# Kernel tuning notes

Hardware: AMD Instinct MI355X
Metric: run time of the kernel (lower is better)

Reference implementation:

```python
import jax, jax.numpy as jnp
import numpy as np

N_NODES = 100000
N_EDGES = 1600000
N_GRAPHS = 2000
F_IN = 64
HID = 64


def setup_inputs() -> dict:
    key = jax.random.key(0)
    ks = jax.random.split(key, 8)
    h = jax.random.normal(ks[0], (N_NODES, F_IN), jnp.float32)
    edge_src = jax.random.randint(ks[1], (N_EDGES,), 0, N_NODES, jnp.int32)
    edge_dst = jax.random.randint(ks[2], (N_EDGES,), 0, N_NODES, jnp.int32)
    graph_ids = jnp.sort(jax.random.randint(ks[3], (N_NODES,), 0, N_GRAPHS, jnp.int32))
    # GraphConv weights (glorot-ish scale) and biases, 3 layers 64->64
    sc = 1.0 / np.sqrt(F_IN)
    W0 = jax.random.normal(ks[4], (F_IN, HID), jnp.float32) * sc
    W1 = jax.random.normal(ks[5], (HID, HID), jnp.float32) * sc
    W2 = jax.random.normal(ks[6], (HID, HID), jnp.float32) * sc
    b0 = jnp.zeros((HID,), jnp.float32)
    b1 = jnp.zeros((HID,), jnp.float32)
    b2 = jnp.zeros((HID,), jnp.float32)
    return dict(h=h, edge_src=edge_src, edge_dst=edge_dst, graph_ids=graph_ids,
                W0=W0, b0=b0, W1=W1, b1=b1, W2=W2, b2=b2)


def _gcn_layer(h, W, b, src, dst, out_deg_isqrt, in_deg_isqrt, apply_relu):
    # DGL GraphConv, norm='both': D_in^{-1/2} A D_out^{-1/2} h W + b
    hw = (h * out_deg_isqrt[:, None]) @ W          # weight/norm commute with sum
    m = jax.ops.segment_sum(hw[src], dst, num_segments=N_NODES)  # gather->scatter-add
    m = m * in_deg_isqrt[:, None] + b
    return jax.nn.relu(m) if apply_relu else m


def reference(h, edge_src, edge_dst, graph_ids, W0, b0, W1, b1, W2, b2):
    ones = jnp.ones((N_EDGES,), h.dtype)
    out_deg = jnp.clip(jax.ops.segment_sum(ones, edge_src, num_segments=N_NODES), 1.0, None)
    in_deg = jnp.clip(jax.ops.segment_sum(ones, edge_dst, num_segments=N_NODES), 1.0, None)
    odi = jax.lax.rsqrt(out_deg)
    idi = jax.lax.rsqrt(in_deg)
    params = [(W0, b0), (W1, b1), (W2, b2)]
    for i, (W, b) in enumerate(params):
        h = _gcn_layer(h, W, b, edge_src, edge_dst, odi, idi, apply_relu=(i < len(params) - 1))
    # self.factor = sqrt(dim) / mean(||h||) computed as python float -> detached constant
    factor = jnp.sqrt(jnp.asarray(HID, h.dtype)) / jnp.mean(jnp.linalg.norm(h, axis=1))
    factor = jax.lax.stop_gradient(factor)
    h = h * factor
    # SumPooling over batched graphs
    return jax.ops.segment_sum(h, graph_ids, num_segments=N_GRAPHS)
```

## Files before the change

kernel.cpp:

```cpp
#include <hip/hip_runtime.h>
#include <hip/hip_fp16.h>

#define N_NODES 100000
#define N_EDGES 1600000
#define N_GRAPHS 2000
#define HID 64
#define NB 391
#define CAP 5120
#define NSUP 16
#define SUPW 6400
#define CAP_S 106496
#define CH_A 2048
#define NCH_A ((N_EDGES + CH_A - 1) / CH_A)
#define BCH 4096
#define NCHB 26
#define GATHER_GRID 2048
#define GEMM_GRID 512
#define N_GROUPS (N_NODES / 4)
#define N_TILE16 (N_NODES / 16)

typedef _Float16 half8 __attribute__((ext_vector_type(8)));
typedef float f32x4 __attribute__((ext_vector_type(4)));

__global__ __launch_bounds__(256) void k_zero2(int* __restrict__ p1, int n1,
                                               int* __restrict__ p2, int n2) {
    int i = blockIdx.x * 256 + threadIdx.x;
    if (i < n1) p1[i] = 0;
    if (i < n2) p2[i] = 0;
}

__global__ __launch_bounds__(256) void k_passA(const int* __restrict__ src, const int* __restrict__ dst,
                                               int* __restrict__ scur_dst, int* __restrict__ scur_src,
                                               unsigned* __restrict__ sup_dst,
                                               unsigned short* __restrict__ sup_src) {
    __shared__ unsigned stD[CH_A];
    __shared__ unsigned short stS[CH_A];
    __shared__ unsigned char binD[CH_A];
    __shared__ unsigned char binS[CH_A];
    __shared__ int lcntD[NSUP], lexD[NSUP], lofD[NSUP], runD[NSUP];
    __shared__ int lcntS[NSUP], lexS[NSUP], lofS[NSUP], runS[NSUP];
    int tid = threadIdx.x;
    int e0 = blockIdx.x * CH_A;
    int n = min(CH_A, N_EDGES - e0);
    if (tid < NSUP) { lcntD[tid] = 0; lcntS[tid] = 0; }
    __syncthreads();
    int sv[8], dv[8];
#pragma unroll
    for (int k = 0; k < 8; ++k) {
        int i = k * 256 + tid;
        if (i < n) { sv[k] = src[e0 + i]; dv[k] = dst[e0 + i]; }
        else dv[k] = -1;
    }
#pragma unroll
    for (int k = 0; k < 8; ++k)
        if (dv[k] >= 0) {
            atomicAdd(&lcntD[dv[k] / SUPW], 1);
            atomicAdd(&lcntS[sv[k] / SUPW], 1);
        }
    __syncthreads();
    if (tid == 0)  { int a = 0; for (int i = 0; i < NSUP; ++i) { lexD[i] = a; lofD[i] = a; a += lcntD[i]; } }
    if (tid == 64) { int a = 0; for (int i = 0; i < NSUP; ++i) { lexS[i] = a; lofS[i] = a; a += lcntS[i]; } }
    __syncthreads();
#pragma unroll
    for (int k = 0; k < 8; ++k)
        if (dv[k] >= 0) {
            int d = dv[k], s = sv[k];
            int bD = d / SUPW;
            int pD = atomicAdd(&lofD[bD], 1);
            stD[pD] = ((unsigned)(d - bD * SUPW) << 17) | (unsigned)s;
            binD[pD] = (unsigned char)bD;
            int bS = s / SUPW;
            int pS = atomicAdd(&lofS[bS], 1);
            stS[pS] = (unsigned short)(s - bS * SUPW);
            binS[pS] = (unsigned char)bS;
        }
    __syncthreads();
    if (tid < NSUP) runD[tid] = lcntD[tid] ? atomicAdd(&scur_dst[tid], lcntD[tid]) : 0;
    if (tid >= 128 && tid < 128 + NSUP) {
        int b = tid - 128;
        runS[b] = lcntS[b] ? atomicAdd(&scur_src[b], lcntS[b]) : 0;
    }
    __syncthreads();
    for (int i = tid; i < n; i += 256) {
        int b = binD[i];
        int pos = runD[b] + (i - lexD[b]);
        if (pos < CAP_S) sup_dst[(size_t)b * CAP_S + pos] = stD[i];
    }
    for (int i = tid; i < n; i += 256) {
        int b = binS[i];
        int pos = runS[b] + (i - lexS[b]);
        if (pos < CAP_S) sup_src[(size_t)b * CAP_S + pos] = stS[i];
    }
}

__global__ __launch_bounds__(256) void k_passB(const unsigned* __restrict__ sup_dst,
                                               const unsigned short* __restrict__ sup_src,
                                               const int* __restrict__ scur_dst,
                                               const int* __restrict__ scur_src,
                                               int* __restrict__ gcur_dst, int* __restrict__ gcur_src,
                                               unsigned* __restrict__ part_dst,
                                               unsigned char* __restrict__ part_src) {
    __shared__ unsigned st[BCH];
    __shared__ unsigned char bin[BCH];
    __shared__ int lcnt[25], lex[25], lof[25], run[25];
    int tid = threadIdx.x;
    int isSrc = blockIdx.x >= NSUP * NCHB;
    int bx = isSrc ? blockIdx.x - NSUP * NCHB : blockIdx.x;
    int sb = bx / NCHB, ch = bx % NCHB;
    int total = isSrc ? scur_src[sb] : scur_dst[sb];
    total = min(total, CAP_S);
    int o0 = ch * BCH;
    int n = min(BCH, total - o0);
    if (n <= 0) return;
    int bg0 = sb * 25;
    if (tid < 25) lcnt[tid] = 0;
    __syncthreads();

    if (!isSrc) {
        unsigned ev[16];
        int bb[16];
#pragma unroll
        for (int k = 0; k < 16; ++k) {
            int i = k * 256 + tid;
            if (i < n) {
                unsigned e = sup_dst[(size_t)sb * CAP_S + o0 + i];
                ev[k] = e;
                bb[k] = (int)(e >> 25);
                atomicAdd(&lcnt[bb[k]], 1);
            } else bb[k] = -1;
        }
        __syncthreads();
        if (tid == 0) { int a = 0; for (int i = 0; i < 25; ++i) { lex[i] = a; lof[i] = a; a += lcnt[i]; } }
        __syncthreads();
#pragma unroll
        for (int k = 0; k < 16; ++k)
            if (bb[k] >= 0) {
                unsigned e = ev[k];
                unsigned s = e & 0x1FFFFu;
                unsigned low = (e >> 17) & 255u;
                int p = atomicAdd(&lof[bb[k]], 1);
                st[p] = (s << 8) | low;
                bin[p] = (unsigned char)bb[k];
            }
        __syncthreads();
        if (tid < 25) run[tid] = lcnt[tid] ? atomicAdd(&gcur_dst[bg0 + tid], lcnt[tid]) : 0;
        __syncthreads();
        for (int i = tid; i < n; i += 256) {
            int b = bin[i];
            int pos = run[b] + (i - lex[b]);
            if (pos < CAP) part_dst[(size_t)(bg0 + b) * CAP + pos] = st[i];
        }
    } else {
        unsigned char* st8 = (unsigned char*)st;
        int rv[16];
        int bb[16];
#pragma unroll
        for (int k = 0; k < 16; ++k) {
            int i = k * 256 + tid;
            if (i < n) {
                int r = (int)sup_src[(size_t)sb * CAP_S + o0 + i];
                rv[k] = r;
                bb[k] = r >> 8;
                atomicAdd(&lcnt[bb[k]], 1);
            } else bb[k] = -1;
        }
        __syncthreads();
        if (tid == 0) { int a = 0; for (int i = 0; i < 25; ++i) { lex[i] = a; lof[i] = a; a += lcnt[i]; } }
        __syncthreads();
#pragma unroll
        for (int k = 0; k < 16; ++k)
            if (bb[k] >= 0) {
                int p = atomicAdd(&lof[bb[k]], 1);
                st8[p] = (unsigned char)(rv[k] & 255);
                bin[p] = (unsigned char)bb[k];
            }
        __syncthreads();
        if (tid < 25) run[tid] = lcnt[tid] ? atomicAdd(&gcur_src[bg0 + tid], lcnt[tid]) : 0;
        __syncthreads();
        for (int i = tid; i < n; i += 256) {
            int b = bin[i];
            int pos = run[b] + (i - lex[b]);
            if (pos < CAP) part_src[(size_t)(bg0 + b) * CAP + pos] = st8[i];
        }
    }
}

__global__ __launch_bounds__(256) void k_csr_count(const unsigned* __restrict__ part_dst,
                                                   const unsigned char* __restrict__ part_src,
                                                   const int* __restrict__ gcur_dst,
                                                   const int* __restrict__ gcur_src,
                                                   int* __restrict__ rowbeg, int* __restrict__ rowend,
                                                   float* __restrict__ idi, float* __restrict__ odi,
                                                   int* __restrict__ col) {
    __shared__ int cnt[256];
    __shared__ int cur[256];
    __shared__ int wsum[4];
    int tid = threadIdx.x;
    if (blockIdx.x >= NB) {
        int b = blockIdx.x - NB;
        int nE = min(gcur_src[b], CAP);
        const unsigned char* pb = part_src + (size_t)b * CAP;
        cnt[tid] = 0;
        __syncthreads();
        for (int i = tid; i < nE; i += 256) atomicAdd(&cnt[pb[i]], 1);
        __syncthreads();
        int v = b * 256 + tid;
        if (v < N_NODES) odi[v] = rsqrtf((float)max(cnt[tid], 1));
        return;
    }
    int b = blockIdx.x;
    int base = b * CAP;
    int nE = min(gcur_dst[b], CAP);
    const unsigned* pb = part_dst + (size_t)b * CAP;
    cnt[tid] = 0;
    __syncthreads();
    for (int i = tid; i < nE; i += 256) atomicAdd(&cnt[pb[i] & 255], 1);
    __syncthreads();
    int c = cnt[tid];
    int incl = c;
#pragma unroll
    for (int off = 1; off < 64; off <<= 1) {
        int t = __shfl_up(incl, off, 64);
        if ((tid & 63) >= off) incl += t;
    }
    if ((tid & 63) == 63) wsum[tid >> 6] = incl;
    __syncthreads();
    int add = 0;
    for (int w = 0; w < (tid >> 6); ++w) add += wsum[w];
    incl += add;
    int excl = incl - c;
    int v = b * 256 + tid;
    if (v < N_NODES) {
        rowbeg[v] = base + excl;
        rowend[v] = base + incl;
        idi[v] = rsqrtf((float)max(c, 1));
    }
    cur[tid] = excl;
    __syncthreads();
    for (int i = tid; i < nE; i += 256) {
        unsigned e = pb[i];
        int p = atomicAdd(&cur[e & 255], 1);
        col[base + p] = (int)(e >> 8);
    }
}

template <int F32IN>
__global__ __launch_bounds__(256) void k_gemm_mfma(const void* __restrict__ inv,
                                                   const float* __restrict__ W,
                                                   const float* __restrict__ odi,
                                                   __half* __restrict__ zs) {
    __shared__ _Float16 Wt[64 * 64];
    int tid = threadIdx.x;
    for (int i = tid; i < 4096; i += 256) {
        int k = i >> 6, j = i & 63;
        Wt[j * 64 + k] = (_Float16)W[i];
    }
    __syncthreads();

    int lane = tid & 63;
    int wid = tid >> 6;
    int lrow = lane & 15;
    int lgrp = lane >> 4;

    half8 Bf[4][2];
#pragma unroll
    for (int nt = 0; nt < 4; ++nt)
#pragma unroll
        for (int kh = 0; kh < 2; ++kh)
            Bf[nt][kh] = *(half8*)&Wt[(nt * 16 + lrow) * 64 + kh * 32 + lgrp * 8];

    for (int t = blockIdx.x * 4 + wid; t < N_TILE16; t += GEMM_GRID * 4) {
        int v0 = t * 16;
        half8 a0, a1;
        if (F32IN) {
            const float* A = (const float*)inv + (size_t)(v0 + lrow) * 64 + lgrp * 8;
            float4 f0 = *(const float4*)A;
            float4 f1 = *(const float4*)(A + 4);
            float4 g0 = *(const float4*)(A + 32);
            float4 g1 = *(const float4*)(A + 36);
            a0[0] = (_Float16)f0.x; a0[1] = (_Float16)f0.y; a0[2] = (_Float16)f0.z; a0[3] = (_Float16)f0.w;
            a0[4] = (_Float16)f1.x; a0[5] = (_Float16)f1.y; a0[6] = (_Float16)f1.z; a0[7] = (_Float16)f1.w;
            a1[0] = (_Float16)g0.x; a1[1] = (_Float16)g0.y; a1[2] = (_Float16)g0.z; a1[3] = (_Float16)g0.w;
            a1[4] = (_Float16)g1.x; a1[5] = (_Float16)g1.y; a1[6] = (_Float16)g1.z; a1[7] = (_Float16)g1.w;
        } else {
            const _Float16* A = (const _Float16*)inv + (size_t)(v0 + lrow) * 64 + lgrp * 8;
            a0 = *(const half8*)A;
            a1 = *(const half8*)(A + 32);
        }
        f32x4 acc[4];
#pragma unroll
        for (int nt = 0; nt < 4; ++nt) { acc[nt] = (f32x4)0.f; }
#pragma unroll
        for (int nt = 0; nt < 4; ++nt) {
            acc[nt] = __builtin_amdgcn_mfma_f32_16x16x32_f16(a0, Bf[nt][0], acc[nt], 0, 0, 0);
            acc[nt] = __builtin_amdgcn_mfma_f32_16x16x32_f16(a1, Bf[nt][1], acc[nt], 0, 0, 0);
        }
#pragma unroll
        for (int r = 0; r < 4; ++r) {
            int node = v0 + lgrp * 4 + r;
            float w = odi[node];
#pragma unroll
            for (int nt = 0; nt < 4; ++nt)
                zs[(size_t)node * 64 + nt * 16 + lrow] = __float2half_rn(acc[nt][r] * w);
        }
    }
}

template <int RELU, int LAST>
__global__ __launch_bounds__(256) void k_gather(const __half* __restrict__ zs, const int* __restrict__ rowbeg,
                                                const int* __restrict__ rowend, const int* __restrict__ col,
                                                const float* __restrict__ idi, const float* __restrict__ b,
                                                __half* __restrict__ xout, float* __restrict__ partials) {
    __shared__ float part[4];
    int tid = threadIdx.x;
    int lane = tid & 63;
    int wid = tid >> 6;
    int half = lane >> 5;
    int fp = lane & 31;
    float2 bias2 = *(const float2*)&b[fp * 2];
    float nacc = 0.f;

    for (int g = blockIdx.x; g < N_GROUPS; g += GATHER_GRID) {
        int v = __builtin_amdgcn_readfirstlane(g * 4 + wid);
        int beg = rowbeg[v], end = rowend[v];
        int deg = end - beg;
        int degS = min(deg, 64);
        int c = col[beg + min(lane, max(degS - 1, 0))];
        float2 a0 = {0.f, 0.f}, a1 = {0.f, 0.f}, a2 = {0.f, 0.f}, a3 = {0.f, 0.f};
        int m = 0;
        for (; (m + 8) * 2 <= degS; m += 8) {
#pragma unroll
            for (int j = 0; j < 8; ++j) {
                int s = __shfl(c, 2 * (m + j) + half, 64);
                float2 f = __half22float2(*((const __half2*)(zs + (size_t)s * 64) + fp));
                if ((j & 3) == 0) { a0.x += f.x; a0.y += f.y; }
                else if ((j & 3) == 1) { a1.x += f.x; a1.y += f.y; }
                else if ((j & 3) == 2) { a2.x += f.x; a2.y += f.y; }
                else { a3.x += f.x; a3.y += f.y; }
            }
        }
        if ((m + 4) * 2 <= degS) {
#pragma unroll
            for (int j = 0; j < 4; ++j) {
                int s = __shfl(c, 2 * (m + j) + half, 64);
                float2 f = __half22float2(*((const __half2*)(zs + (size_t)s * 64) + fp));
                if (j == 0) { a0.x += f.x; a0.y += f.y; }
                else if (j == 1) { a1.x += f.x; a1.y += f.y; }
                else if (j == 2) { a2.x += f.x; a2.y += f.y; }
                else { a3.x += f.x; a3.y += f.y; }
            }
            m += 4;
        }
        if (m * 2 < degS) {
#pragma unroll
            for (int j = 0; j < 4; ++j) {
                int e = 2 * (m + j) + half;
                int ee = (e < degS) ? e : (degS - 1);
                int s = __shfl(c, ee, 64);
                float2 f = __half22float2(*((const __half2*)(zs + (size_t)s * 64) + fp));
                float msk = (e < degS) ? 1.f : 0.f;
                if (j == 0) { a0.x = fmaf(f.x, msk, a0.x); a0.y = fmaf(f.y, msk, a0.y); }
                else if (j == 1) { a1.x = fmaf(f.x, msk, a1.x); a1.y = fmaf(f.y, msk, a1.y); }
                else if (j == 2) { a2.x = fmaf(f.x, msk, a2.x); a2.y = fmaf(f.y, msk, a2.y); }
                else { a3.x = fmaf(f.x, msk, a3.x); a3.y = fmaf(f.y, msk, a3.y); }
            }
        }
        if (deg > 64) {
            for (int p = beg + 64; p < end; p += 8) {
#pragma unroll
                for (int j = 0; j < 4; ++j) {
                    int e = p + 2 * j + half;
                    int q = (e < end) ? e : (end - 1);
                    int s = col[q];
                    float2 f = __half22float2(*((const __half2*)(zs + (size_t)s * 64) + fp));
                    float msk = (e < end) ? 1.f : 0.f;
                    a0.x = fmaf(f.x, msk, a0.x); a0.y = fmaf(f.y, msk, a0.y);
                }
            }
        }
        float2 a;
        a.x = (a0.x + a1.x) + (a2.x + a3.x);
        a.y = (a0.y + a1.y) + (a2.y + a3.y);
        a.x += __shfl_xor(a.x, 32, 64);
        a.y += __shfl_xor(a.y, 32, 64);
        float iv = idi[v];
        float2 o;
        o.x = fmaf(a.x, iv, bias2.x);
        o.y = fmaf(a.y, iv, bias2.y);
        if (RELU) { o.x = fmaxf(o.x, 0.f); o.y = fmaxf(o.y, 0.f); }

        if (half == 0)
            *((__half2*)(xout + (size_t)v * 64) + fp) = __floats2half2_rn(o.x, o.y);

        if (LAST) {
            float s = o.x * o.x + o.y * o.y;
#pragma unroll
            for (int off = 32; off > 0; off >>= 1) s += __shfl_xor(s, off, 64);
            if (lane == 0) nacc += sqrtf(0.5f * s);
        }
    }

    if (LAST) {
        if (lane == 0) part[wid] = nacc;
        __syncthreads();
        if (tid == 0) partials[blockIdx.x] = part[0] + part[1] + part[2] + part[3];
    }
}

__global__ __launch_bounds__(256) void k_reduce_factor(const float* __restrict__ partials,
                                                       float* __restrict__ factor) {
    __shared__ float sd[256];
    int tid = threadIdx.x;
    float s = 0.f;
    for (int i = tid; i < GATHER_GRID; i += 256) s += partials[i];
    sd[tid] = s;
    __syncthreads();
    for (int off = 128; off > 0; off >>= 1) {
        if (tid < off) sd[tid] += sd[tid + off];
        __syncthreads();
    }
    if (tid == 0) factor[0] = 8.0f * (float)N_NODES / sd[0];
}

#define POOL_CHUNK 32
__global__ __launch_bounds__(256) void k_pool(const __half* __restrict__ h, const int* __restrict__ gid,
                                              const float* __restrict__ factor, float* __restrict__ out) {
    int wave = (blockIdx.x * 256 + threadIdx.x) >> 6;
    int lane = threadIdx.x & 63;
    int v0 = wave * POOL_CHUNK;
    if (v0 >= N_NODES) return;
    float f = factor[0];
    int vend = min(v0 + POOL_CHUNK, N_NODES);
    int gprev = gid[v0];
    float acc = 0.f;
    for (int v = v0; v < vend; ++v) {
        int g = gid[v];
        if (g != gprev) {
            atomicAdd(&out[(size_t)gprev * 64 + lane], acc);
            acc = 0.f;
            gprev = g;
        }
        acc = fmaf(__half2float(h[(size_t)v * 64 + lane]), f, acc);
    }
    atomicAdd(&out[(size_t)gprev * 64 + lane], acc);
}

extern "C" void kernel_launch(void* const* d_in, const int* in_sizes, int n_in,
                              void* d_out, int out_size, void* d_ws, size_t ws_size,
                              hipStream_t stream) {
    const float* h    = (const float*)d_in[0];
    const int*   esrc = (const int*)d_in[1];
    const int*   edst = (const int*)d_in[2];
    const int*   gids = (const int*)d_in[3];
    const float* W0 = (const float*)d_in[4];
    const float* b0 = (const float*)d_in[5];
    const float* W1 = (const float*)d_in[6];
    const float* b1 = (const float*)d_in[7];
    const float* W2 = (const float*)d_in[8];
    const float* b2 = (const float*)d_in[9];
    float* out = (float*)d_out;

    char* wsp = (char*)d_ws;
    size_t off = 0;
    auto alloc = [&](size_t bytes) -> void* {
        void* p = wsp + off;
        off += (bytes + 255) & ~(size_t)255;
        return p;
    };
    int*   cursors    = (int*)alloc(814 * 4);
    float* odi        = (float*)alloc((size_t)N_NODES * 4);
    float* idi        = (float*)alloc((size_t)N_NODES * 4);
    int*   rowbeg     = (int*)alloc((size_t)N_NODES * 4);
    int*   rowend     = (int*)alloc((size_t)N_NODES * 4);
    float* partials   = (float*)alloc((size_t)GATHER_GRID * 4);
    float* factor     = (float*)alloc(4);
    int*   col        = (int*)alloc((size_t)NB * CAP * 4);
    __half* zsb       = (__half*)alloc((size_t)N_NODES * 64 * 2);
    __half* xh        = (__half*)alloc((size_t)N_NODES * 64 * 2);
    unsigned*       sup_dst  = (unsigned*)alloc((size_t)NSUP * CAP_S * 4);
    unsigned short* sup_src  = (unsigned short*)alloc((size_t)NSUP * CAP_S * 2);
    unsigned*       part_dst = (unsigned*)alloc((size_t)NB * CAP * 4);
    unsigned char*  part_src = (unsigned char*)alloc((size_t)NB * CAP);

    int* scur_dst = cursors;
    int* scur_src = cursors + 16;
    int* gcur_dst = cursors + 32;
    int* gcur_src = cursors + 32 + NB;

    k_zero2<<<(N_GRAPHS * 64 + 255) / 256, 256, 0, stream>>>(cursors, 814, (int*)out, N_GRAPHS * 64);

    k_passA<<<NCH_A, 256, 0, stream>>>(esrc, edst, scur_dst, scur_src, sup_dst, sup_src);
    k_passB<<<2 * NSUP * NCHB, 256, 0, stream>>>(sup_dst, sup_src, scur_dst, scur_src,
                                                 gcur_dst, gcur_src, part_dst, part_src);
    k_csr_count<<<2 * NB, 256, 0, stream>>>(part_dst, part_src, gcur_dst, gcur_src,
                                            rowbeg, rowend, idi, odi, col);

    k_gemm_mfma<1><<<GEMM_GRID, 256, 0, stream>>>(h, W0, odi, zsb);
    k_gather<1, 0><<<GATHER_GRID, 256, 0, stream>>>(zsb, rowbeg, rowend, col, idi, b0, xh, nullptr);
    k_gemm_mfma<0><<<GEMM_GRID, 256, 0, stream>>>(xh, W1, odi, zsb);
    k_gather<1, 0><<<GATHER_GRID, 256, 0, stream>>>(zsb, rowbeg, rowend, col, idi, b1, xh, nullptr);
    k_gemm_mfma<0><<<GEMM_GRID, 256, 0, stream>>>(xh, W2, odi, zsb);
    k_gather<0, 1><<<GATHER_GRID, 256, 0, stream>>>(zsb, rowbeg, rowend, col, idi, b2, xh, partials);

    k_reduce_factor<<<1, 256, 0, stream>>>(partials, factor);
    int poolWaves  = (N_NODES + POOL_CHUNK - 1) / POOL_CHUNK;
    int poolBlocks = (poolWaves + 3) / 4;
    k_pool<<<poolBlocks, 256, 0, stream>>>(xh, gids, factor, out);
}
```

Measured before the change: 206.5 us.

## Fuse sum pooling into last gather layer and scale output in finish kernel

The final aggregation layer now adds its per-node outputs directly into per-graph accumulators with atomics, instead of writing fp16 node features for a separate pooling kernel to read back. Because pooling is linear, the norm factor is applied afterwards by a finish kernel in which every block redundantly reduces the partial norms and scales its slice of the output. Every gather layer also switches from interleaved 4-node groups to contiguous 13-node runs per wave, which lets consecutive nodes of one graph share an accumulator. The cost is some load imbalance from the fixed chunks and a small repeated reduction in each finish block.

```diff
diff --git a/kernel.cpp b/kernel.cpp
--- a/kernel.cpp
+++ b/kernel.cpp
@@ -15,8 +15,8 @@
 #define BCH 4096
 #define NCHB 26
 #define GATHER_GRID 2048
+#define NPW 13
 #define GEMM_GRID 512
-#define N_GROUPS (N_NODES / 4)
 #define N_TILE16 (N_NODES / 16)
 
 typedef _Float16 half8 __attribute__((ext_vector_type(8)));
@@ -310,7 +310,8 @@
 __global__ __launch_bounds__(256) void k_gather(const __half* __restrict__ zs, const int* __restrict__ rowbeg,
                                                 const int* __restrict__ rowend, const int* __restrict__ col,
                                                 const float* __restrict__ idi, const float* __restrict__ b,
-                                                __half* __restrict__ xout, float* __restrict__ partials) {
+                                                __half* __restrict__ xout, const int* __restrict__ gid,
+                                                float* __restrict__ out, float* __restrict__ partials) {
     __shared__ float part[4];
     int tid = threadIdx.x;
     int lane = tid & 63;
@@ -319,9 +320,14 @@
     int fp = lane & 31;
     float2 bias2 = *(const float2*)&b[fp * 2];
     float nacc = 0.f;
-
-    for (int g = blockIdx.x; g < N_GROUPS; g += GATHER_GRID) {
-        int v = __builtin_amdgcn_readfirstlane(g * 4 + wid);
+    float2 pacc = {0.f, 0.f};
+    int curg = -1;
+
+    int w = __builtin_amdgcn_readfirstlane(blockIdx.x * 4 + wid);
+    int v0 = w * NPW;
+    int vend = min(v0 + NPW, N_NODES);
+
+    for (int v = v0; v < vend; ++v) {
         int beg = rowbeg[v], end = rowend[v];
         int deg = end - beg;
         int degS = min(deg, 64);
@@ -389,26 +395,40 @@
         o.y = fmaf(a.y, iv, bias2.y);
         if (RELU) { o.x = fmaxf(o.x, 0.f); o.y = fmaxf(o.y, 0.f); }
 
-        if (half == 0)
-            *((__half2*)(xout + (size_t)v * 64) + fp) = __floats2half2_rn(o.x, o.y);
-
         if (LAST) {
+            int gg = gid[v];
+            if (gg != curg) {
+                if (curg >= 0 && half == 0) {
+                    atomicAdd(&out[(size_t)curg * 64 + fp * 2], pacc.x);
+                    atomicAdd(&out[(size_t)curg * 64 + fp * 2 + 1], pacc.y);
+                }
+                curg = gg;
+                pacc.x = 0.f; pacc.y = 0.f;
+            }
+            pacc.x += o.x; pacc.y += o.y;
             float s = o.x * o.x + o.y * o.y;
 #pragma unroll
             for (int off = 32; off > 0; off >>= 1) s += __shfl_xor(s, off, 64);
             if (lane == 0) nacc += sqrtf(0.5f * s);
+        } else {
+            if (half == 0)
+                *((__half2*)(xout + (size_t)v * 64) + fp) = __floats2half2_rn(o.x, o.y);
         }
     }
 
     if (LAST) {
+        if (curg >= 0 && half == 0) {
+            atomicAdd(&out[(size_t)curg * 64 + fp * 2], pacc.x);
+            atomicAdd(&out[(size_t)curg * 64 + fp * 2 + 1], pacc.y);
+        }
         if (lane == 0) part[wid] = nacc;
         __syncthreads();
         if (tid == 0) partials[blockIdx.x] = part[0] + part[1] + part[2] + part[3];
     }
 }
 
-__global__ __launch_bounds__(256) void k_reduce_factor(const float* __restrict__ partials,
-                                                       float* __restrict__ factor) {
+__global__ __launch_bounds__(256) void k_finish(const float* __restrict__ partials,
+                                                float* __restrict__ out) {
     __shared__ float sd[256];
     int tid = threadIdx.x;
     float s = 0.f;
@@ -419,30 +439,9 @@
         if (tid < off) sd[tid] += sd[tid + off];
         __syncthreads();
     }
-    if (tid == 0) factor[0] = 8.0f * (float)N_NODES / sd[0];
-}
-
-#define POOL_CHUNK 32
-__global__ __launch_bounds__(256) void k_pool(const __half* __restrict__ h, const int* __restrict__ gid,
-                                              const float* __restrict__ factor, float* __restrict__ out) {
-    int wave = (blockIdx.x * 256 + threadIdx.x) >> 6;
-    int lane = threadIdx.x & 63;
-    int v0 = wave * POOL_CHUNK;
-    if (v0 >= N_NODES) return;
-    float f = factor[0];
-    int vend = min(v0 + POOL_CHUNK, N_NODES);
-    int gprev = gid[v0];
-    float acc = 0.f;
-    for (int v = v0; v < vend; ++v) {
-        int g = gid[v];
-        if (g != gprev) {
-            atomicAdd(&out[(size_t)gprev * 64 + lane], acc);
-            acc = 0.f;
-            gprev = g;
-        }
-        acc = fmaf(__half2float(h[(size_t)v * 64 + lane]), f, acc);
-    }
-    atomicAdd(&out[(size_t)gprev * 64 + lane], acc);
+    float factor = 8.0f * (float)N_NODES / sd[0];
+    int i = blockIdx.x * 256 + tid;
+    if (i < N_GRAPHS * 64) out[i] *= factor;
 }
 
 extern "C" void kernel_launch(void* const* d_in, const int* in_sizes, int n_in,
@@ -473,7 +472,6 @@
     int*   rowbeg     = (int*)alloc((size_t)N_NODES * 4);
     int*   rowend     = (int*)alloc((size_t)N_NODES * 4);
     float* partials   = (float*)alloc((size_t)GATHER_GRID * 4);
-    float* factor     = (float*)alloc(4);
     int*   col        = (int*)alloc((size_t)NB * CAP * 4);
     __half* zsb       = (__half*)alloc((size_t)N_NODES * 64 * 2);
     __half* xh        = (__half*)alloc((size_t)N_NODES * 64 * 2);
@@ -496,14 +494,14 @@
                                             rowbeg, rowend, idi, odi, col);
 
     k_gemm_mfma<1><<<GEMM_GRID, 256, 0, stream>>>(h, W0, odi, zsb);
-    k_gather<1, 0><<<GATHER_GRID, 256, 0, stream>>>(zsb, rowbeg, rowend, col, idi, b0, xh, nullptr);
+    k_gather<1, 0><<<GATHER_GRID, 256, 0, stream>>>(zsb, rowbeg, rowend, col, idi, b0, xh,
+                                                    nullptr, nullptr, nullptr);
     k_gemm_mfma<0><<<GEMM_GRID, 256, 0, stream>>>(xh, W1, odi, zsb);
-    k_gather<1, 0><<<GATHER_GRID, 256, 0, stream>>>(zsb, rowbeg, rowend, col, idi, b1, xh, nullptr);
+    k_gather<1, 0><<<GATHER_GRID, 256, 0, stream>>>(zsb, rowbeg, rowend, col, idi, b1, xh,
+                                                    nullptr, nullptr, nullptr);
     k_gemm_mfma<0><<<GEMM_GRID, 256, 0, stream>>>(xh, W2, odi, zsb);
-    k_gather<0, 1><<<GATHER_GRID, 256, 0, stream>>>(zsb, rowbeg, rowend, col, idi, b2, xh, partials);
-
-    k_reduce_factor<<<1, 256, 0, stream>>>(partials, factor);
-    int poolWaves  = (N_NODES + POOL_CHUNK - 1) / POOL_CHUNK;
-    int poolBlocks = (poolWaves + 3) / 4;
-    k_pool<<<poolBlocks, 256, 0, stream>>>(xh, gids, factor, out);
-}
+    k_gather<0, 1><<<GATHER_GRID, 256, 0, stream>>>(zsb, rowbeg, rowend, col, idi, b2, nullptr,
+                                                    gids, out, partials);
+
+    k_finish<<<(N_GRAPHS * 64 + 255) / 256, 256, 0, stream>>>(partials, out);
+}
```

Result: faster. 194.1 us (median of 2 runs) (-6.0%).
